# Kernel tuning notes

Hardware: AMD Instinct MI355X
Metric: run time of the kernel (lower is better)

Reference implementation:

```python
import jax, jax.numpy as jnp
import numpy as np

B, Z, A, D = 2048, 128, 4, 50000
EPS = 1e-8


def setup_inputs() -> dict:
    key = jax.random.key(0)
    k1, k2, k3, k4, k5 = jax.random.split(key, 5)
    return {
        "batch_x": jax.random.normal(k1, (B, Z), dtype=jnp.float32),
        "batch_next": jax.random.normal(k2, (B, Z), dtype=jnp.float32),
        "keys": jax.random.normal(k3, (A, D, Z), dtype=jnp.float32),
        "vals": jax.random.normal(k4, (A, D, Z), dtype=jnp.float32),
        "batch_a": jax.random.randint(k5, (B,), 0, A, dtype=jnp.int64),
    }


def _dnd_lookup(q, keys_a, vals_a):
    # q: [B, Z] (L2-normalized), keys_a: [D, Z], vals_a: [D, Z]
    kn = keys_a / (jnp.linalg.norm(keys_a, axis=-1, keepdims=True) + EPS)
    sims = jnp.einsum("bz,dz->bd", q, kn)          # cosine similarity [B, D]
    w = jax.nn.softmax(sims, axis=-1)                # attention over dictionary
    return jnp.einsum("bd,dz->bz", w, vals_a)       # [B, Z]


def reference(batch_x, batch_next, keys, vals, batch_a):
    # Per-sample routed DND lookup: each sample queries the memory of its action,
    # then MSE loss vs batch_next (eval-mode trainBatch; memory write is a state
    # mutation done after the loss and does not affect the returned value).
    qn = batch_x / (jnp.linalg.norm(batch_x, axis=-1, keepdims=True) + EPS)
    a_space = keys.shape[0]
    pred = jnp.zeros_like(batch_x)
    for a in range(a_space):  # small fixed loop over distinct memories
        pred_a = _dnd_lookup(qn, keys[a], vals[a])
        pred = jnp.where((batch_a == a)[:, None], pred_a, pred)
    return jnp.mean((pred - batch_next) ** 2)
```

## Files before the change

### kernel.cpp

```cpp
#include <hip/hip_runtime.h>
#include <stdint.h>

#define B_N 2048
#define Z_N 128
#define A_N 4
#define D_N 50000
#define D_PAD 51200
#define EPS_F 1e-8f

#define TILE_B 128
#define KT 32
#define NSPLIT 64
#define SPAN 800
#define NITER 25
#define KL_S 140
#define VL_S 40

typedef __attribute__((ext_vector_type(8))) short short8;
typedef __attribute__((ext_vector_type(4))) float f32x4;
typedef __attribute__((ext_vector_type(2))) unsigned int u32x2;

__device__ __forceinline__ unsigned short f2bf(float f) {
  unsigned int u = __builtin_bit_cast(unsigned int, f);
  u += 0x7FFFu + ((u >> 16) & 1u);
  return (unsigned short)(u >> 16);
}

__device__ __forceinline__ void plswap32(unsigned int& a, unsigned int& b) {
#if __has_builtin(__builtin_amdgcn_permlane32_swap)
  u32x2 r = __builtin_amdgcn_permlane32_swap(a, b, false, false);
  a = r[0]; b = r[1];
#else
  asm volatile("v_permlane32_swap_b32 %0, %1" : "+v"(a), "+v"(b));
#endif
}
__device__ __forceinline__ void plswap16(unsigned int& a, unsigned int& b) {
#if __has_builtin(__builtin_amdgcn_permlane16_swap)
  u32x2 r = __builtin_amdgcn_permlane16_swap(a, b, false, false);
  a = r[0]; b = r[1];
#else
  asm volatile("v_permlane16_swap_b32 %0, %1" : "+v"(a), "+v"(b));
#endif
}

__global__ void k_norm(const float* __restrict__ keys, const float* __restrict__ x,
                       unsigned short* __restrict__ kn, unsigned short* __restrict__ qnb) {
  int w = threadIdx.x >> 6, lane = threadIdx.x & 63;
  int row = blockIdx.x * 4 + w;
  const float* src;
  unsigned short* dst;
  if (row >= A_N * D_PAD) {
    int r = row - A_N * D_PAD;
    src = x + (size_t)r * Z_N;
    dst = qnb + (size_t)r * Z_N;
  } else {
    int a = row / D_PAD, d = row - a * D_PAD;
    dst = kn + (size_t)row * Z_N;
    if (d >= D_N) { ((unsigned int*)dst)[lane] = 0u; return; }
    src = keys + ((size_t)a * D_N + d) * Z_N;
  }
  const float2 v = ((const float2*)src)[lane];
  float ss = v.x * v.x + v.y * v.y;
#pragma unroll
  for (int m = 1; m < 64; m <<= 1) ss += __shfl_xor(ss, m);
  float inv = 1.0f / (sqrtf(ss) + EPS_F);
  unsigned int packed = ((unsigned int)f2bf(v.y * inv) << 16) | f2bf(v.x * inv);
  ((unsigned int*)dst)[lane] = packed;
}

__global__ void k_vtrans(const float* __restrict__ vals, unsigned short* __restrict__ vt) {
  __shared__ float tile[64][65];
  int a = blockIdx.z, d0 = blockIdx.x * 64, z0 = blockIdx.y * 64;
  int t = threadIdx.x;
  int r = t >> 4, c4 = (t & 15) * 4;
#pragma unroll
  for (int i = 0; i < 4; ++i) {
    int dr = r + i * 16, d = d0 + dr;
    float4 v = {0.f, 0.f, 0.f, 0.f};
    if (d < D_N) v = *(const float4*)(vals + ((size_t)a * D_N + d) * Z_N + z0 + c4);
    tile[dr][c4 + 0] = v.x; tile[dr][c4 + 1] = v.y;
    tile[dr][c4 + 2] = v.z; tile[dr][c4 + 3] = v.w;
  }
  __syncthreads();
  int zz = t >> 2, dg = (t & 3) * 16;
  union { unsigned short u[16]; uint4 q[2]; } pk;
#pragma unroll
  for (int j = 0; j < 16; ++j) pk.u[j] = f2bf(tile[dg + j][zz]);
  unsigned short* dst = vt + ((size_t)a * Z_N + z0 + zz) * D_PAD + d0 + dg;
  ((uint4*)dst)[0] = pk.q[0];
  ((uint4*)dst)[1] = pk.q[1];
}

__global__ void k_route(const int* __restrict__ act, int* __restrict__ counts,
                        int* __restrict__ lists, int* __restrict__ work) {
  __shared__ int lc[4];
  int t = threadIdx.x;
  if (t < 4) lc[t] = 0;
  __syncthreads();
  for (int i = t; i < B_N; i += 1024) {
    int a = act[i];
    int pos = atomicAdd(&lc[a], 1);
    lists[a * B_N + pos] = i;
  }
  __syncthreads();
  if (t < 4) counts[t] = lc[t];
  int t0 = (lc[0] + TILE_B - 1) >> 7, t1 = (lc[1] + TILE_B - 1) >> 7;
  int t2 = (lc[2] + TILE_B - 1) >> 7, t3 = (lc[3] + TILE_B - 1) >> 7;
  int T = t0 + t1 + t2 + t3;
  int total = T * NSPLIT;
  if (t == 0) work[0] = total;
  for (int i = t; i < total; i += 1024) {
    int lo = i & 7, q = i >> 3;
    int chi = q / T, j = q - chi * T;
    int c = (chi << 3) | lo;
    int a, ty;
    if (j < t0)                { a = 0; ty = j; }
    else if (j < t0 + t1)      { a = 1; ty = j - t0; }
    else if (j < t0 + t1 + t2) { a = 2; ty = j - t0 - t1; }
    else                       { a = 3; ty = j - t0 - t1 - t2; }
    work[1 + i] = a | (ty << 2) | (c << 8);
  }
}

__launch_bounds__(512)
__global__ void k_flash(const unsigned short* __restrict__ kn,
                        const unsigned short* __restrict__ vt,
                        const unsigned short* __restrict__ qnb,
                        const int* __restrict__ counts,
                        const int* __restrict__ lists,
                        const int* __restrict__ work,
                        float* __restrict__ acc,
                        float* __restrict__ sume) {
  int total = work[0];
  if ((int)blockIdx.x >= total) return;
  int wi = work[1 + blockIdx.x];
  int a = wi & 3, ty = (wi >> 2) & 63, span = wi >> 8;
  int nb = counts[a];

  __shared__ unsigned short Kl[2][KT * KL_S];
  __shared__ unsigned short Vl[2][128 * VL_S];

  int t = threadIdx.x;
  int w = t >> 6, lane = t & 63;
  int lq = lane >> 4, ln = lane & 15;

  const unsigned short* kn_a = kn + (size_t)a * D_PAD * Z_N;
  const unsigned short* vt_a = vt + (size_t)a * Z_N * D_PAD;
  const int* list_a = lists + a * B_N;

  int g0 = ty * TILE_B + w * 16 + ln;
  bool qvalid = g0 < nb;
  int si0 = qvalid ? list_a[g0] : 0;
  short8 qf[4];
#pragma unroll
  for (int c = 0; c < 4; ++c) {
    short8 s = (short8){0,0,0,0,0,0,0,0};
    if (qvalid) s = *(const short8*)(qnb + (size_t)si0 * Z_N + c * 32 + lq * 8);
    qf[c] = s;
  }

  f32x4 O[8];
#pragma unroll
  for (int zt = 0; zt < 8; ++zt) O[zt] = (f32x4){0.f, 0.f, 0.f, 0.f};
  float rs = 0.f;

  int d_base = span * SPAN;
  int sk_key = t >> 4, sk_z = (t & 15) * 8;
  int sv_z = t >> 2, sv_k = (t & 3) * 8;

  uint4 kp, vp;

#define LOAD_TILE(d)                                                          \
  {                                                                           \
    kp = *(const uint4*)(kn_a + (size_t)((d) + sk_key) * Z_N + sk_z);         \
    vp = *(const uint4*)(vt_a + (size_t)sv_z * D_PAD + (d) + sv_k);           \
  }
#define STORE_TILE(p)                                                         \
  {                                                                           \
    *(uint4*)&Kl[p][sk_key * KL_S + sk_z] = kp;                               \
    *(uint4*)&Vl[p][sv_z * VL_S + sv_k] = vp;                                 \
  }

  LOAD_TILE(d_base);
  STORE_TILE(0);
  LOAD_TILE(d_base + KT);
  __syncthreads();

  int p = 0;
  for (int kt = 0; kt < NITER; ++kt) {
    int d0 = d_base + kt * KT;
    if (kt + 1 < NITER) {
      STORE_TILE(p ^ 1);
      if (kt + 2 < NITER) LOAD_TILE(d0 + 2 * KT)
    }

    f32x4 ST[2];
#pragma unroll
    for (int nt = 0; nt < 2; ++nt) {
      short8 kf[4];
#pragma unroll
      for (int c = 0; c < 4; ++c)
        kf[c] = *(const short8*)&Kl[p][(nt * 16 + ln) * KL_S + c * 32 + lq * 8];
      f32x4 s4 = (f32x4){0.f, 0.f, 0.f, 0.f};
#pragma unroll
      for (int c = 0; c < 4; ++c)
        s4 = __builtin_amdgcn_mfma_f32_16x16x32_bf16(kf[c], qf[c], s4, 0, 0, 0);
      ST[nt] = s4;
    }

    unsigned int s00, s01, s10, s11;
#pragma unroll
    for (int nt = 0; nt < 2; ++nt) {
      float e0 = __expf(ST[nt][0]);
      float e1 = __expf(ST[nt][1]);
      float e2 = __expf(ST[nt][2]);
      float e3 = __expf(ST[nt][3]);
      rs += (e0 + e1) + (e2 + e3);
      unsigned int lo, hi;
      asm("v_cvt_pk_bf16_f32 %0, %1, %2" : "=v"(lo) : "v"(e0), "v"(e1));
      asm("v_cvt_pk_bf16_f32 %0, %1, %2" : "=v"(hi) : "v"(e2), "v"(e3));
      if (nt == 0) { s00 = lo; s01 = hi; } else { s10 = lo; s11 = hi; }
    }

    plswap32(s00, s10);
    plswap32(s01, s11);
    plswap16(s00, s10);
    plswap16(s01, s11);
    union { unsigned int u[4]; short8 v; } pa;
    pa.u[0] = s00; pa.u[1] = s01; pa.u[2] = s10; pa.u[3] = s11;

#pragma unroll
    for (int zt = 0; zt < 8; ++zt) {
      short8 vf = *(const short8*)&Vl[p][(zt * 16 + ln) * VL_S + lq * 8];
      O[zt] = __builtin_amdgcn_mfma_f32_16x16x32_bf16(pa.v, vf, O[zt], 0, 0, 0);
    }

    __syncthreads();
    p ^= 1;
  }

  rs += __shfl_xor(rs, 16);
  rs += __shfl_xor(rs, 32);

  if (lq == 0 && qvalid) atomicAdd(&sume[si0], rs);
#pragma unroll
  for (int r = 0; r < 4; ++r) {
    int g = ty * TILE_B + w * 16 + lq * 4 + r;
    if (g < nb) {
      int si = list_a[g];
      float* arow = acc + (size_t)si * Z_N + ln;
#pragma unroll
      for (int zt = 0; zt < 8; ++zt) atomicAdd(arow + zt * 16, O[zt][r]);
    }
  }
}

__global__ void k_loss(const float* __restrict__ acc, const float* __restrict__ sume,
                       const float* __restrict__ nxt, float* __restrict__ loss) {
  __shared__ float ls[4];
  int w = threadIdx.x >> 6, lane = threadIdx.x & 63;
  int row = blockIdx.x * 4 + w;
  float inv = 1.0f / (sume[row] - (float)(D_PAD - D_N));
  const float2 p2 = ((const float2*)(acc + (size_t)row * Z_N))[lane];
  const float2 n2 = ((const float2*)(nxt + (size_t)row * Z_N))[lane];
  float dx = p2.x * inv - n2.x, dy = p2.y * inv - n2.y;
  float s = dx * dx + dy * dy;
#pragma unroll
  for (int m = 1; m < 64; m <<= 1) s += __shfl_xor(s, m);
  if (lane == 0) ls[w] = s;
  __syncthreads();
  if (threadIdx.x == 0) atomicAdd(loss, ls[0] + ls[1] + ls[2] + ls[3]);
}

__global__ void k_final(const float* __restrict__ loss, float* __restrict__ out) {
  out[0] = loss[0] * (1.0f / (float)(B_N * Z_N));
}

extern "C" void kernel_launch(void* const* d_in, const int* in_sizes, int n_in,
                              void* d_out, int out_size, void* d_ws, size_t ws_size,
                              hipStream_t stream) {
  const float* x    = (const float*)d_in[0];
  const float* nxt  = (const float*)d_in[1];
  const float* keys = (const float*)d_in[2];
  const float* vals = (const float*)d_in[3];
  const int*   act  = (const int*)d_in[4];

  char* ws = (char*)d_ws;
  float* acc    = (float*)(ws + 0);
  float* sume   = (float*)(ws + 1048576);
  float* loss   = (float*)(ws + 1056768);
  int*   counts = (int*)(ws + 1056784);
  int*   lists  = (int*)(ws + 1056800);
  int*   work   = (int*)(ws + 1089568);
  unsigned short* qnb = (unsigned short*)(ws + 1097760);
  unsigned short* kn  = (unsigned short*)(ws + 1622048);
  unsigned short* vt  = (unsigned short*)(ws + 54050848);

  hipMemsetAsync(ws, 0, 1056784, stream);

  k_norm<<<51712, 256, 0, stream>>>(keys, x, kn, qnb);
  k_vtrans<<<dim3(800, 2, A_N), 256, 0, stream>>>(vals, vt);
  k_route<<<1, 1024, 0, stream>>>(act, counts, lists, work);
  k_flash<<<1216, 512, 0, stream>>>(kn, vt, qnb, counts, lists, work, acc, sume);
  k_loss<<<512, 256, 0, stream>>>(acc, sume, nxt, loss);
  k_final<<<1, 1, 0, stream>>>(loss, (float*)d_out);
}
```

Baseline: 385.0 us.

## Merge prep kernels, fold final scaling into loss, add MFMA priority hints

Fuses the key/query normalisation kernel and the value transpose kernel into one launch. It also removes the final scaling kernel by having the loss kernel atomically add pre-scaled partial sums straight into the output, which is zeroed with a memset. Inside the flash loop it raises wave priority around the MFMA blocks and flattens the exp/pack loop. The main aim is fewer kernel launches and less inter-kernel idle time, plus better MFMA issue. The cost is a kernel with branchy dual roles, an extra memset, and a summation order for the loss that changes slightly.

Result: slower. 392.9 us (+2.1%).

```diff
diff --git a/kernel.cpp b/kernel.cpp
--- a/kernel.cpp
+++ b/kernel.cpp
@@ -16,6 +16,9 @@
 #define KL_S 140
 #define VL_S 40
 
+#define NORM_BLOCKS 51712
+#define VT_BX 800
+
 typedef __attribute__((ext_vector_type(8))) short short8;
 typedef __attribute__((ext_vector_type(4))) float f32x4;
 typedef __attribute__((ext_vector_type(2))) unsigned int u32x2;
@@ -43,34 +46,39 @@
 #endif
 }
 
-__global__ void k_norm(const float* __restrict__ keys, const float* __restrict__ x,
-                       unsigned short* __restrict__ kn, unsigned short* __restrict__ qnb) {
-  int w = threadIdx.x >> 6, lane = threadIdx.x & 63;
-  int row = blockIdx.x * 4 + w;
-  const float* src;
-  unsigned short* dst;
-  if (row >= A_N * D_PAD) {
-    int r = row - A_N * D_PAD;
-    src = x + (size_t)r * Z_N;
-    dst = qnb + (size_t)r * Z_N;
-  } else {
-    int a = row / D_PAD, d = row - a * D_PAD;
-    dst = kn + (size_t)row * Z_N;
-    if (d >= D_N) { ((unsigned int*)dst)[lane] = 0u; return; }
-    src = keys + ((size_t)a * D_N + d) * Z_N;
-  }
-  const float2 v = ((const float2*)src)[lane];
-  float ss = v.x * v.x + v.y * v.y;
-#pragma unroll
-  for (int m = 1; m < 64; m <<= 1) ss += __shfl_xor(ss, m);
-  float inv = 1.0f / (sqrtf(ss) + EPS_F);
-  unsigned int packed = ((unsigned int)f2bf(v.y * inv) << 16) | f2bf(v.x * inv);
-  ((unsigned int*)dst)[lane] = packed;
-}
-
-__global__ void k_vtrans(const float* __restrict__ vals, unsigned short* __restrict__ vt) {
+__global__ void k_prep(const float* __restrict__ keys, const float* __restrict__ x,
+                       const float* __restrict__ vals,
+                       unsigned short* __restrict__ kn, unsigned short* __restrict__ qnb,
+                       unsigned short* __restrict__ vt) {
+  if (blockIdx.x < NORM_BLOCKS) {
+    int w = threadIdx.x >> 6, lane = threadIdx.x & 63;
+    int row = blockIdx.x * 4 + w;
+    const float* src;
+    unsigned short* dst;
+    if (row >= A_N * D_PAD) {
+      int r = row - A_N * D_PAD;
+      src = x + (size_t)r * Z_N;
+      dst = qnb + (size_t)r * Z_N;
+    } else {
+      int a = row / D_PAD, d = row - a * D_PAD;
+      dst = kn + (size_t)row * Z_N;
+      if (d >= D_N) { ((unsigned int*)dst)[lane] = 0u; return; }
+      src = keys + ((size_t)a * D_N + d) * Z_N;
+    }
+    const float2 v = ((const float2*)src)[lane];
+    float ss = v.x * v.x + v.y * v.y;
+#pragma unroll
+    for (int m = 1; m < 64; m <<= 1) ss += __shfl_xor(ss, m);
+    float inv = 1.0f / (sqrtf(ss) + EPS_F);
+    unsigned int packed = ((unsigned int)f2bf(v.y * inv) << 16) | f2bf(v.x * inv);
+    ((unsigned int*)dst)[lane] = packed;
+    return;
+  }
   __shared__ float tile[64][65];
-  int a = blockIdx.z, d0 = blockIdx.x * 64, z0 = blockIdx.y * 64;
+  int b = blockIdx.x - NORM_BLOCKS;
+  int bx = b % VT_BX, rest = b / VT_BX;
+  int by = rest & 1, a = rest >> 1;
+  int d0 = bx * 64, z0 = by * 64;
   int t = threadIdx.x;
   int r = t >> 4, c4 = (t & 15) * 4;
 #pragma unroll
@@ -195,6 +203,7 @@
     }
 
     f32x4 ST[2];
+    __builtin_amdgcn_s_setprio(1);
 #pragma unroll
     for (int nt = 0; nt < 2; ++nt) {
       short8 kf[4];
@@ -207,19 +216,19 @@
         s4 = __builtin_amdgcn_mfma_f32_16x16x32_bf16(kf[c], qf[c], s4, 0, 0, 0);
       ST[nt] = s4;
     }
+    __builtin_amdgcn_s_setprio(0);
 
     unsigned int s00, s01, s10, s11;
-#pragma unroll
-    for (int nt = 0; nt < 2; ++nt) {
-      float e0 = __expf(ST[nt][0]);
-      float e1 = __expf(ST[nt][1]);
-      float e2 = __expf(ST[nt][2]);
-      float e3 = __expf(ST[nt][3]);
-      rs += (e0 + e1) + (e2 + e3);
-      unsigned int lo, hi;
-      asm("v_cvt_pk_bf16_f32 %0, %1, %2" : "=v"(lo) : "v"(e0), "v"(e1));
-      asm("v_cvt_pk_bf16_f32 %0, %1, %2" : "=v"(hi) : "v"(e2), "v"(e3));
-      if (nt == 0) { s00 = lo; s01 = hi; } else { s10 = lo; s11 = hi; }
+    {
+      float e0 = __expf(ST[0][0]), e1 = __expf(ST[0][1]);
+      float e2 = __expf(ST[0][2]), e3 = __expf(ST[0][3]);
+      float f0 = __expf(ST[1][0]), f1 = __expf(ST[1][1]);
+      float f2 = __expf(ST[1][2]), f3 = __expf(ST[1][3]);
+      rs += ((e0 + e1) + (e2 + e3)) + ((f0 + f1) + (f2 + f3));
+      asm("v_cvt_pk_bf16_f32 %0, %1, %2" : "=v"(s00) : "v"(e0), "v"(e1));
+      asm("v_cvt_pk_bf16_f32 %0, %1, %2" : "=v"(s01) : "v"(e2), "v"(e3));
+      asm("v_cvt_pk_bf16_f32 %0, %1, %2" : "=v"(s10) : "v"(f0), "v"(f1));
+      asm("v_cvt_pk_bf16_f32 %0, %1, %2" : "=v"(s11) : "v"(f2), "v"(f3));
     }
 
     plswap32(s00, s10);
@@ -229,11 +238,13 @@
     union { unsigned int u[4]; short8 v; } pa;
     pa.u[0] = s00; pa.u[1] = s01; pa.u[2] = s10; pa.u[3] = s11;
 
+    __builtin_amdgcn_s_setprio(1);
 #pragma unroll
     for (int zt = 0; zt < 8; ++zt) {
       short8 vf = *(const short8*)&Vl[p][(zt * 16 + ln) * VL_S + lq * 8];
       O[zt] = __builtin_amdgcn_mfma_f32_16x16x32_bf16(pa.v, vf, O[zt], 0, 0, 0);
     }
+    __builtin_amdgcn_s_setprio(0);
 
     __syncthreads();
     p ^= 1;
@@ -256,7 +267,7 @@
 }
 
 __global__ void k_loss(const float* __restrict__ acc, const float* __restrict__ sume,
-                       const float* __restrict__ nxt, float* __restrict__ loss) {
+                       const float* __restrict__ nxt, float* __restrict__ out) {
   __shared__ float ls[4];
   int w = threadIdx.x >> 6, lane = threadIdx.x & 63;
   int row = blockIdx.x * 4 + w;
@@ -269,11 +280,8 @@
   for (int m = 1; m < 64; m <<= 1) s += __shfl_xor(s, m);
   if (lane == 0) ls[w] = s;
   __syncthreads();
-  if (threadIdx.x == 0) atomicAdd(loss, ls[0] + ls[1] + ls[2] + ls[3]);
-}
-
-__global__ void k_final(const float* __restrict__ loss, float* __restrict__ out) {
-  out[0] = loss[0] * (1.0f / (float)(B_N * Z_N));
+  if (threadIdx.x == 0)
+    atomicAdd(out, (ls[0] + ls[1] + ls[2] + ls[3]) * (1.0f / (float)(B_N * Z_N)));
 }
 
 extern "C" void kernel_launch(void* const* d_in, const int* in_sizes, int n_in,
@@ -288,7 +296,6 @@
   char* ws = (char*)d_ws;
   float* acc    = (float*)(ws + 0);
   float* sume   = (float*)(ws + 1048576);
-  float* loss   = (float*)(ws + 1056768);
   int*   counts = (int*)(ws + 1056784);
   int*   lists  = (int*)(ws + 1056800);
   int*   work   = (int*)(ws + 1089568);
@@ -297,11 +304,10 @@
   unsigned short* vt  = (unsigned short*)(ws + 54050848);
 
   hipMemsetAsync(ws, 0, 1056784, stream);
-
-  k_norm<<<51712, 256, 0, stream>>>(keys, x, kn, qnb);
-  k_vtrans<<<dim3(800, 2, A_N), 256, 0, stream>>>(vals, vt);
+  hipMemsetAsync(d_out, 0, 4, stream);
+
   k_route<<<1, 1024, 0, stream>>>(act, counts, lists, work);
+  k_prep<<<NORM_BLOCKS + VT_BX * 2 * A_N, 256, 0, stream>>>(keys, x, vals, kn, qnb, vt);
   k_flash<<<1216, 512, 0, stream>>>(kn, vt, qnb, counts, lists, work, acc, sume);
-  k_loss<<<512, 256, 0, stream>>>(acc, sume, nxt, loss);
-  k_final<<<1, 1, 0, stream>>>(loss, (float*)d_out);
-}
+  k_loss<<<512, 256, 0, stream>>>(acc, sume, nxt, (float*)d_out);
+}
```
